# Performance work log

Measured on AMD Instinct MI355X. Metric: run time of the kernel, lower is better.

Reference implementation:

```python
import jax, jax.numpy as jnp
import numpy as np

DT_MIN, DT_MAX, STAB_EPS, RMS_EPS = 1e-4, 10.0, 1e-8, 1e-6


def soft_clamp(x, mn=DT_MIN, mx=DT_MAX):
    center = (mx + mn) / 2.0
    half = (mx - mn) / 2.0
    return center + half * jnp.tanh((x - center) / half)


def setup_inputs() -> dict:
    key = jax.random.key(0)
    ks = jax.random.split(key, 8)
    B, L, D, N = 1, 4096, 1024, 16
    s = D ** -0.5
    x = jax.random.normal(ks[0], (B, L, D), jnp.float32)
    # S4D-real style init: A = -exp(A_log), rows = -(1..N)
    A_log = jnp.broadcast_to(jnp.log(jnp.arange(1, N + 1, dtype=jnp.float32)), (D, N))
    W_delta = jax.random.normal(ks[1], (D, D), jnp.float32) * s
    b_delta = jax.random.normal(ks[2], (D,), jnp.float32) * 0.1
    W_B = jax.random.normal(ks[3], (D, N), jnp.float32) * s
    W_C = jax.random.normal(ks[4], (D, N), jnp.float32) * s
    D_skip = jax.random.normal(ks[5], (D,), jnp.float32) * 0.1 + 1.0
    norm_weight = jnp.ones((D,), jnp.float32)
    return {"x": x, "A_log": A_log, "W_delta": W_delta, "b_delta": b_delta,
            "W_B": W_B, "W_C": W_C, "D_skip": D_skip, "norm_weight": norm_weight}


def reference(x, A_log, W_delta, b_delta, W_B, W_C, D_skip, norm_weight):
    # RMSNorm pre-norm
    rms = jnp.sqrt(jnp.mean(x * x, axis=-1, keepdims=True) + RMS_EPS)
    xn = norm_weight * x / rms                                  # (B, L, D)

    # input-dependent (selective) parameters
    delta = soft_clamp(jax.nn.softplus(xn @ W_delta + b_delta))  # (B, L, D)
    Bp = xn @ W_B                                               # (B, L, N)
    C = xn @ W_C                                                # (B, L, N)
    A = -jnp.exp(A_log)                                         # (D, N)

    # guarded Tustin (bilinear) discretization
    half_dA = 0.5 * delta[..., None] * A                        # (B, L, D, N)
    denom_inv = 1.0 / jnp.maximum(1.0 - half_dA, STAB_EPS)
    A_bar = (1.0 + half_dA) * denom_inv                         # (B, L, D, N)
    B_bar = jnp.sqrt(delta)[..., None] * Bp[:, :, None, :] * denom_inv
    Bx = B_bar * xn[..., None]                                  # (B, L, D, N)

    # linear recurrence h_t = A_bar_t * h_{t-1} + Bx_t ; y_t = sum_n C_t * h_t
    def step(h, inp):
        a_t, bx_t, c_t = inp
        h = a_t * h + bx_t                                      # (B, D, N)
        y_t = jnp.einsum('bdn,bn->bd', h, c_t)
        return h, y_t

    h0 = jnp.zeros((x.shape[0], A.shape[0], A.shape[1]), x.dtype)
    seq = (jnp.moveaxis(A_bar, 1, 0), jnp.moveaxis(Bx, 1, 0), jnp.moveaxis(C, 1, 0))
    _, ys = jax.lax.scan(step, h0, seq)
    y = jnp.moveaxis(ys, 0, 1) + D_skip * xn                    # skip connection
    return y
```

## Files before the change

kernel.cpp:

```cpp
#include <hip/hip_runtime.h>
#include <hip/hip_fp16.h>
#include <cmath>

typedef _Float16 half8 __attribute__((ext_vector_type(8)));
typedef _Float16 half4_t __attribute__((ext_vector_type(4)));
typedef _Float16 half2_t __attribute__((ext_vector_type(2)));
typedef float f32x4 __attribute__((ext_vector_type(4)));
typedef float f32x2 __attribute__((ext_vector_type(2)));

#define LDIM 4096
#define DDIM 1024
#define NSTATE 16
#define NCHUNK 128
#define CLEN 32

#define GLD16(g, l) __builtin_amdgcn_global_load_lds( \
    (const __attribute__((address_space(1))) void*)(g), \
    (__attribute__((address_space(3))) void*)(l), 16, 0, 0)

__global__ __launch_bounds__(256) void k_prep_norm(const float* __restrict__ x,
                                                   const float* __restrict__ nw,
                                                   const float* __restrict__ W,
                                                   const float* __restrict__ WB,
                                                   const float* __restrict__ WC,
                                                   _Float16* __restrict__ xnh,
                                                   _Float16* __restrict__ Wt,
                                                   _Float16* __restrict__ BCe) {
  const int b = blockIdx.x, t = threadIdx.x;
  if (b < 4096) {
    const int l = b;
    float4 v = ((const float4*)(x + (size_t)l * DDIM))[t];
    float ss = v.x * v.x + v.y * v.y + v.z * v.z + v.w * v.w;
#pragma unroll
    for (int off = 32; off; off >>= 1) ss += __shfl_xor(ss, off, 64);
    __shared__ float sred[4];
    if ((t & 63) == 0) sred[t >> 6] = ss;
    __syncthreads();
    float tot = sred[0] + sred[1] + sred[2] + sred[3];
    float r = rsqrtf(tot * (1.0f / (float)DDIM) + 1e-6f);
    float4 wv = ((const float4*)nw)[t];
    half4_t h;
    h[0] = (_Float16)(v.x * wv.x * r); h[1] = (_Float16)(v.y * wv.y * r);
    h[2] = (_Float16)(v.z * wv.z * r); h[3] = (_Float16)(v.w * wv.w * r);
    ((half4_t*)(xnh + (size_t)l * DDIM))[t] = h;
  } else if (b < 4352) {
    __shared__ float tile[64][65];
    const int bb = b - 4096;
    const int n0 = (bb & 15) * 64, k0 = (bb >> 4) * 64;
#pragma unroll
    for (int i = 0; i < 16; ++i) {
      int idx = t + i * 256;
      int kk = idx >> 6, nn = idx & 63;
      tile[kk][nn] = W[(size_t)(k0 + kk) * DDIM + n0 + nn];
    }
    __syncthreads();
#pragma unroll
    for (int i = 0; i < 16; ++i) {
      int idx = t + i * 256;
      int nn = idx >> 6, kk = idx & 63;
      Wt[(size_t)(n0 + nn) * DDIM + k0 + kk] = (_Float16)tile[kk][nn];
    }
  } else {
    const int by2 = b - 4352;
#pragma unroll
    for (int rr = 0; rr < 2; ++rr) {
      int r = 2 * by2 + rr;
      const float* src = (r < 16) ? WB : WC;
      int n = r & 15;
#pragma unroll
      for (int j = 0; j < 4; ++j) {
        int k = t * 4 + j;
        BCe[(size_t)r * DDIM + k] = (_Float16)src[(size_t)k * NSTATE + n];
      }
    }
  }
}

__global__ __launch_bounds__(256, 2) void k_gemm64(const _Float16* __restrict__ Ah,
                                                   const _Float16* __restrict__ Bh,
                                                   const _Float16* __restrict__ B2h,
                                                   const float* __restrict__ b_delta,
                                                   half2_t* __restrict__ sxh,
                                                   float* __restrict__ bpc) {
  __shared__ __align__(16) _Float16 As[2][128 * 64];
  __shared__ __align__(16) _Float16 Bs[2][64 * 64];
  __shared__ __align__(16) _Float16 B2s[2][32 * 64];
  const int t = threadIdx.x;
  const int w = t >> 6, lane = t & 63;
  const int quad = lane >> 4, l16 = lane & 15;
  const int wr = w >> 1, wc = w & 1;
  const int bid = blockIdx.x;
  const int bx = bid & 15, by = bid >> 4;
  const int tileM = by * 128, tileN = bx * 64;
  const int srow = lane >> 3;
  const int sslot = (lane & 7) ^ srow;
  const _Float16* gA0 = Ah + (size_t)(tileM + w * 32 + srow) * DDIM + sslot * 8;
  const _Float16* gB0 = Bh + (size_t)(tileN + w * 16 + srow) * DDIM + sslot * 8;
  const _Float16* gC0 = B2h + (size_t)(w * 8 + srow) * DDIM + sslot * 8;

  f32x4 acc[4][2], acc2[4];
#pragma unroll
  for (int i = 0; i < 4; ++i) {
    acc2[i] = (f32x4){0.f, 0.f, 0.f, 0.f};
#pragma unroll
    for (int j = 0; j < 2; ++j) acc[i][j] = (f32x4){0.f, 0.f, 0.f, 0.f};
  }

  auto stage = [&](int kt, int p) {
    const int ko = kt * 64;
#pragma unroll
    for (int g = 0; g < 4; ++g)
      GLD16(gA0 + (size_t)g * 8 * DDIM + ko, &As[p][(w * 32 + g * 8) * 64]);
#pragma unroll
    for (int g = 0; g < 2; ++g)
      GLD16(gB0 + (size_t)g * 8 * DDIM + ko, &Bs[p][(w * 16 + g * 8) * 64]);
    if (bx == 0)
      GLD16(gC0 + ko, &B2s[p][(w * 8) * 64]);
  };

  stage(0, 0);
  for (int kt = 0; kt < 16; ++kt) {
    const int p = kt & 1;
    __syncthreads();
    if (kt < 15) stage(kt + 1, p ^ 1);
#pragma unroll
    for (int ks = 0; ks < 2; ++ks) {
      const int sw = ((ks * 4 + quad) ^ (l16 & 7)) * 8;
      half8 af[4], bf[2];
#pragma unroll
      for (int i = 0; i < 4; ++i)
        af[i] = *(const half8*)&As[p][(wr * 64 + i * 16 + l16) * 64 + sw];
#pragma unroll
      for (int j = 0; j < 2; ++j)
        bf[j] = *(const half8*)&Bs[p][(wc * 32 + j * 16 + l16) * 64 + sw];
#pragma unroll
      for (int i = 0; i < 4; ++i)
#pragma unroll
        for (int j = 0; j < 2; ++j)
          acc[i][j] = __builtin_amdgcn_mfma_f32_16x16x32_f16(af[i], bf[j], acc[i][j], 0, 0, 0);
      if (bx == 0) {
        half8 cf = *(const half8*)&B2s[p][(wc * 16 + l16) * 64 + sw];
#pragma unroll
        for (int i = 0; i < 4; ++i)
          acc2[i] = __builtin_amdgcn_mfma_f32_16x16x32_f16(af[i], cf, acc2[i], 0, 0, 0);
      }
    }
  }

  const float cC = 5.00005f, cH = 4.99995f, invH = 1.0f / 4.99995f;
  float bdl[2];
#pragma unroll
  for (int j = 0; j < 2; ++j) bdl[j] = b_delta[tileN + wc * 32 + j * 16 + l16];
#pragma unroll
  for (int i = 0; i < 4; ++i) {
#pragma unroll
    for (int r = 0; r < 4; ++r) {
      int row = tileM + wr * 64 + i * 16 + quad * 4 + r;
#pragma unroll
      for (int j = 0; j < 2; ++j) {
        int col = tileN + wc * 32 + j * 16 + l16;
        float z = acc[i][j][r] + bdl[j];
        float e = __expf(-fabsf(z));
        float sp = fmaxf(z, 0.f) + __logf(1.0f + e);
        float tt = (sp - cC) * invH;
        float e2 = __expf(2.0f * tt);
        float th = 1.0f - 2.0f * __builtin_amdgcn_rcpf(e2 + 1.0f);
        float dt = fmaf(cH, th, cC);
        half2_t pk;
        pk[0] = (_Float16)sqrtf(dt);
        pk[1] = Ah[(size_t)row * DDIM + col];
        sxh[(size_t)row * DDIM + col] = pk;
      }
      if (bx == 0)
        bpc[(size_t)row * 32 + wc * 16 + l16] = acc2[i][r];
    }
  }
}

__global__ __launch_bounds__(256) void k_scan1(const half2_t* __restrict__ sxh,
                                               const float* __restrict__ bpc,
                                               const float* __restrict__ A_log,
                                               float2* __restrict__ Ph) {
  const int t = threadIdx.x;
  const int d = blockIdx.x * 256 + t;
  const int c = blockIdx.y;
  const float4* alp = (const float4*)(A_log + (size_t)d * NSTATE);
  f32x2 halfA[8], h[8], P[8];
#pragma unroll
  for (int q = 0; q < 4; ++q) {
    float4 al = alp[q];
    halfA[2 * q + 0] = (f32x2){-0.5f * __expf(al.x), -0.5f * __expf(al.y)};
    halfA[2 * q + 1] = (f32x2){-0.5f * __expf(al.z), -0.5f * __expf(al.w)};
  }
#pragma unroll
  for (int j = 0; j < 8; ++j) { h[j] = (f32x2){0.f, 0.f}; P[j] = (f32x2){1.f, 1.f}; }
  const half2_t* sxr = sxh + (size_t)c * CLEN * DDIM + d;
  const float* bp0 = bpc + (size_t)c * CLEN * 32;
  const f32x2 one2 = {1.f, 1.f}, two2 = {2.f, 2.f}, mone2 = {-1.f, -1.f};
#pragma unroll 4
  for (int i = 0; i < CLEN; ++i) {
    half2_t sx = sxr[(size_t)i * DDIM];
    float sdv = (float)sx[0], xv = (float)sx[1];
    float dsq = sdv * sdv, sdx = sdv * xv;
    f32x2 dsq2 = {dsq, dsq}, sdx2 = {sdx, sdx};
    const float* bp = bp0 + i * 32;
#pragma unroll
    for (int j = 0; j < 8; ++j) {
      f32x2 bB = *(const f32x2*)(bp + 2 * j);
      f32x2 hd = dsq2 * halfA[j];
      f32x2 om = one2 - hd;
      f32x2 di = {__builtin_amdgcn_rcpf(om[0]), __builtin_amdgcn_rcpf(om[1])};
      f32x2 ab = __builtin_elementwise_fma(di, two2, mone2);
      h[j] = __builtin_elementwise_fma(ab, h[j], sdx2 * bB * di);
      P[j] = P[j] * ab;
    }
  }
#pragma unroll
  for (int j = 0; j < 8; ++j) {
    Ph[((size_t)c * NSTATE + 2 * j + 0) * DDIM + d] = make_float2(P[j][0], h[j][0]);
    Ph[((size_t)c * NSTATE + 2 * j + 1) * DDIM + d] = make_float2(P[j][1], h[j][1]);
  }
}

__global__ __launch_bounds__(64) void k_comb(const float2* __restrict__ Ph,
                                             float* __restrict__ Hinit) {
  const int g = blockIdx.x * 64 + threadIdx.x;
  float H = 0.f;
  for (int cb = 0; cb < NCHUNK; cb += 16) {
    float2 ph[16];
#pragma unroll
    for (int u = 0; u < 16; ++u)
      ph[u] = Ph[(size_t)(cb + u) * (DDIM * NSTATE) + g];
#pragma unroll
    for (int u = 0; u < 16; ++u) {
      Hinit[(size_t)(cb + u) * (DDIM * NSTATE) + g] = H;
      H = fmaf(ph[u].x, H, ph[u].y);
    }
  }
}

__global__ __launch_bounds__(256) void k_scan2(const half2_t* __restrict__ sxh,
                                               const float* __restrict__ bpc,
                                               const float* __restrict__ A_log,
                                               const float* __restrict__ Hinit,
                                               const float* __restrict__ Dskip,
                                               float* __restrict__ y) {
  const int t = threadIdx.x;
  const int d = blockIdx.x * 256 + t;
  const int c = blockIdx.y;
  const float4* alp = (const float4*)(A_log + (size_t)d * NSTATE);
  f32x2 halfA[8], h[8];
#pragma unroll
  for (int q = 0; q < 4; ++q) {
    float4 al = alp[q];
    halfA[2 * q + 0] = (f32x2){-0.5f * __expf(al.x), -0.5f * __expf(al.y)};
    halfA[2 * q + 1] = (f32x2){-0.5f * __expf(al.z), -0.5f * __expf(al.w)};
  }
#pragma unroll
  for (int j = 0; j < 8; ++j)
    h[j] = (f32x2){Hinit[(size_t)c * (DDIM * NSTATE) + (size_t)(2 * j) * DDIM + d],
                   Hinit[(size_t)c * (DDIM * NSTATE) + (size_t)(2 * j + 1) * DDIM + d]};
  const float dsk = Dskip[d];
  const half2_t* sxr = sxh + (size_t)c * CLEN * DDIM + d;
  const float* bp0 = bpc + (size_t)c * CLEN * 32;
  float* yr = y + (size_t)c * CLEN * DDIM + d;
  const f32x2 one2 = {1.f, 1.f}, two2 = {2.f, 2.f}, mone2 = {-1.f, -1.f};
#pragma unroll 4
  for (int i = 0; i < CLEN; ++i) {
    half2_t sx = sxr[(size_t)i * DDIM];
    float sdv = (float)sx[0], xv = (float)sx[1];
    float dsq = sdv * sdv, sdx = sdv * xv;
    f32x2 dsq2 = {dsq, dsq}, sdx2 = {sdx, sdx};
    const float* bp = bp0 + i * 32;
    f32x2 acc = {0.f, 0.f};
#pragma unroll
    for (int j = 0; j < 8; ++j) {
      f32x2 bB = *(const f32x2*)(bp + 2 * j);
      f32x2 bC = *(const f32x2*)(bp + 16 + 2 * j);
      f32x2 hd = dsq2 * halfA[j];
      f32x2 om = one2 - hd;
      f32x2 di = {__builtin_amdgcn_rcpf(om[0]), __builtin_amdgcn_rcpf(om[1])};
      f32x2 ab = __builtin_elementwise_fma(di, two2, mone2);
      h[j] = __builtin_elementwise_fma(ab, h[j], sdx2 * bB * di);
      acc = __builtin_elementwise_fma(bC, h[j], acc);
    }
    yr[(size_t)i * DDIM] = fmaf(dsk, xv, acc[0] + acc[1]);
  }
}

extern "C" void kernel_launch(void* const* d_in, const int* in_sizes, int n_in,
                              void* d_out, int out_size, void* d_ws, size_t ws_size,
                              hipStream_t stream) {
  const float* x       = (const float*)d_in[0];
  const float* A_log   = (const float*)d_in[1];
  const float* W_delta = (const float*)d_in[2];
  const float* b_delta = (const float*)d_in[3];
  const float* W_B     = (const float*)d_in[4];
  const float* W_C     = (const float*)d_in[5];
  const float* D_skip  = (const float*)d_in[6];
  const float* norm_w  = (const float*)d_in[7];
  float* y = (float*)d_out;

  char* ws = (char*)d_ws;
  const size_t MB = 1024 * 1024;
  _Float16* xnh = (_Float16*)(ws);
  _Float16* Wt  = (_Float16*)(ws + 8 * MB);
  _Float16* BCe = (_Float16*)(ws + 10 * MB);
  float*    bpc = (float*)(ws + 10 * MB + 512 * 1024);
  half2_t*  sxh = (half2_t*)(ws + 11 * MB);
  float2*   Ph  = (float2*)(ws + 27 * MB);
  float*    Hin = (float*)(ws + 43 * MB);
  (void)ws_size; (void)in_sizes; (void)n_in; (void)out_size;

  hipLaunchKernelGGL(k_prep_norm, dim3(4368), dim3(256), 0, stream,
                     x, norm_w, W_delta, W_B, W_C, xnh, Wt, BCe);
  hipLaunchKernelGGL(k_gemm64, dim3(512), dim3(256), 0, stream,
                     xnh, Wt, BCe, b_delta, sxh, bpc);
  hipLaunchKernelGGL(k_scan1, dim3(4, NCHUNK), dim3(256), 0, stream,
                     sxh, bpc, A_log, Ph);
  hipLaunchKernelGGL(k_comb, dim3(256), dim3(64), 0, stream, Ph, Hin);
  hipLaunchKernelGGL(k_scan2, dim3(4, NCHUNK), dim3(256), 0, stream,
                     sxh, bpc, A_log, Hin, D_skip, y);
}
```

Baseline: 159.5 us.

## Split scan state across four lanes per channel and stage B/C in LDS

The chunked scan kernels now give each channel four threads, each owning four of the sixteen states, which quadruples the thread count (16x128 blocks) and cuts per-thread serial work and registers. The per-chunk B/C projections are staged once into shared memory instead of being read from global memory by every thread. In the second scan, partial outputs are reduced across the four lanes with shuffles. The GEMM block index is also remapped so consecutive blocks share the same N tile across eight M tiles, aiming for better L2 reuse. The cost is redundant sxh loads (four lanes read the same value), extra shuffles per step, and more, smaller blocks.

```diff
diff --git a/kernel.cpp b/kernel.cpp
--- a/kernel.cpp
+++ b/kernel.cpp
@@ -90,7 +90,8 @@
   const int quad = lane >> 4, l16 = lane & 15;
   const int wr = w >> 1, wc = w & 1;
   const int bid = blockIdx.x;
-  const int bx = bid & 15, by = bid >> 4;
+  const int bx = bid >> 5;
+  const int by = (bid & 7) + ((bid >> 3) & 3) * 8;
   const int tileM = by * 128, tileN = bx * 64;
   const int srow = lane >> 3;
   const int sslot = (lane & 7) ^ srow;
@@ -177,25 +178,24 @@
   }
 }
 
-__global__ __launch_bounds__(256) void k_scan1(const half2_t* __restrict__ sxh,
-                                               const float* __restrict__ bpc,
-                                               const float* __restrict__ A_log,
-                                               float2* __restrict__ Ph) {
+__global__ __launch_bounds__(256, 8) void k_scan1(const half2_t* __restrict__ sxh,
+                                                  const float* __restrict__ bpc,
+                                                  const float* __restrict__ A_log,
+                                                  float2* __restrict__ Ph) {
+  __shared__ __align__(16) float bcs[CLEN * 32];
   const int t = threadIdx.x;
-  const int d = blockIdx.x * 256 + t;
+  const int q = t & 3;
+  const int d = blockIdx.x * 64 + (t >> 2);
   const int c = blockIdx.y;
-  const float4* alp = (const float4*)(A_log + (size_t)d * NSTATE);
-  f32x2 halfA[8], h[8], P[8];
-#pragma unroll
-  for (int q = 0; q < 4; ++q) {
-    float4 al = alp[q];
-    halfA[2 * q + 0] = (f32x2){-0.5f * __expf(al.x), -0.5f * __expf(al.y)};
-    halfA[2 * q + 1] = (f32x2){-0.5f * __expf(al.z), -0.5f * __expf(al.w)};
-  }
-#pragma unroll
-  for (int j = 0; j < 8; ++j) { h[j] = (f32x2){0.f, 0.f}; P[j] = (f32x2){1.f, 1.f}; }
+  ((float4*)bcs)[t] = ((const float4*)(bpc + (size_t)c * CLEN * 32))[t];
+  float4 al = *(const float4*)(A_log + (size_t)d * NSTATE + q * 4);
+  f32x2 halfA[2], h[2], P[2];
+  halfA[0] = (f32x2){-0.5f * __expf(al.x), -0.5f * __expf(al.y)};
+  halfA[1] = (f32x2){-0.5f * __expf(al.z), -0.5f * __expf(al.w)};
+  h[0] = h[1] = (f32x2){0.f, 0.f};
+  P[0] = P[1] = (f32x2){1.f, 1.f};
+  __syncthreads();
   const half2_t* sxr = sxh + (size_t)c * CLEN * DDIM + d;
-  const float* bp0 = bpc + (size_t)c * CLEN * 32;
   const f32x2 one2 = {1.f, 1.f}, two2 = {2.f, 2.f}, mone2 = {-1.f, -1.f};
 #pragma unroll 4
   for (int i = 0; i < CLEN; ++i) {
@@ -203,22 +203,22 @@
     float sdv = (float)sx[0], xv = (float)sx[1];
     float dsq = sdv * sdv, sdx = sdv * xv;
     f32x2 dsq2 = {dsq, dsq}, sdx2 = {sdx, sdx};
-    const float* bp = bp0 + i * 32;
-#pragma unroll
-    for (int j = 0; j < 8; ++j) {
-      f32x2 bB = *(const f32x2*)(bp + 2 * j);
+    f32x4 bB = *(const f32x4*)&bcs[i * 32 + q * 4];
+#pragma unroll
+    for (int j = 0; j < 2; ++j) {
+      f32x2 bb = (f32x2){bB[2 * j], bB[2 * j + 1]};
       f32x2 hd = dsq2 * halfA[j];
       f32x2 om = one2 - hd;
       f32x2 di = {__builtin_amdgcn_rcpf(om[0]), __builtin_amdgcn_rcpf(om[1])};
       f32x2 ab = __builtin_elementwise_fma(di, two2, mone2);
-      h[j] = __builtin_elementwise_fma(ab, h[j], sdx2 * bB * di);
+      h[j] = __builtin_elementwise_fma(ab, h[j], sdx2 * bb * di);
       P[j] = P[j] * ab;
     }
   }
 #pragma unroll
-  for (int j = 0; j < 8; ++j) {
-    Ph[((size_t)c * NSTATE + 2 * j + 0) * DDIM + d] = make_float2(P[j][0], h[j][0]);
-    Ph[((size_t)c * NSTATE + 2 * j + 1) * DDIM + d] = make_float2(P[j][1], h[j][1]);
+  for (int j = 0; j < 2; ++j) {
+    Ph[((size_t)c * NSTATE + q * 4 + 2 * j + 0) * DDIM + d] = make_float2(P[j][0], h[j][0]);
+    Ph[((size_t)c * NSTATE + q * 4 + 2 * j + 1) * DDIM + d] = make_float2(P[j][1], h[j][1]);
   }
 }
 
@@ -239,30 +239,28 @@
   }
 }
 
-__global__ __launch_bounds__(256) void k_scan2(const half2_t* __restrict__ sxh,
-                                               const float* __restrict__ bpc,
-                                               const float* __restrict__ A_log,
-                                               const float* __restrict__ Hinit,
-                                               const float* __restrict__ Dskip,
-                                               float* __restrict__ y) {
+__global__ __launch_bounds__(256, 8) void k_scan2(const half2_t* __restrict__ sxh,
+                                                  const float* __restrict__ bpc,
+                                                  const float* __restrict__ A_log,
+                                                  const float* __restrict__ Hinit,
+                                                  const float* __restrict__ Dskip,
+                                                  float* __restrict__ y) {
+  __shared__ __align__(16) float bcs[CLEN * 32];
   const int t = threadIdx.x;
-  const int d = blockIdx.x * 256 + t;
+  const int q = t & 3;
+  const int d = blockIdx.x * 64 + (t >> 2);
   const int c = blockIdx.y;
-  const float4* alp = (const float4*)(A_log + (size_t)d * NSTATE);
-  f32x2 halfA[8], h[8];
-#pragma unroll
-  for (int q = 0; q < 4; ++q) {
-    float4 al = alp[q];
-    halfA[2 * q + 0] = (f32x2){-0.5f * __expf(al.x), -0.5f * __expf(al.y)};
-    halfA[2 * q + 1] = (f32x2){-0.5f * __expf(al.z), -0.5f * __expf(al.w)};
-  }
-#pragma unroll
-  for (int j = 0; j < 8; ++j)
-    h[j] = (f32x2){Hinit[(size_t)c * (DDIM * NSTATE) + (size_t)(2 * j) * DDIM + d],
-                   Hinit[(size_t)c * (DDIM * NSTATE) + (size_t)(2 * j + 1) * DDIM + d]};
+  ((float4*)bcs)[t] = ((const float4*)(bpc + (size_t)c * CLEN * 32))[t];
+  float4 al = *(const float4*)(A_log + (size_t)d * NSTATE + q * 4);
+  f32x2 halfA[2], h[2];
+  halfA[0] = (f32x2){-0.5f * __expf(al.x), -0.5f * __expf(al.y)};
+  halfA[1] = (f32x2){-0.5f * __expf(al.z), -0.5f * __expf(al.w)};
+  const float* hb = Hinit + (size_t)c * (DDIM * NSTATE) + d;
+  h[0] = (f32x2){hb[(size_t)(q * 4 + 0) * DDIM], hb[(size_t)(q * 4 + 1) * DDIM]};
+  h[1] = (f32x2){hb[(size_t)(q * 4 + 2) * DDIM], hb[(size_t)(q * 4 + 3) * DDIM]};
   const float dsk = Dskip[d];
+  __syncthreads();
   const half2_t* sxr = sxh + (size_t)c * CLEN * DDIM + d;
-  const float* bp0 = bpc + (size_t)c * CLEN * 32;
   float* yr = y + (size_t)c * CLEN * DDIM + d;
   const f32x2 one2 = {1.f, 1.f}, two2 = {2.f, 2.f}, mone2 = {-1.f, -1.f};
 #pragma unroll 4
@@ -271,20 +269,24 @@
     float sdv = (float)sx[0], xv = (float)sx[1];
     float dsq = sdv * sdv, sdx = sdv * xv;
     f32x2 dsq2 = {dsq, dsq}, sdx2 = {sdx, sdx};
-    const float* bp = bp0 + i * 32;
+    f32x4 bB = *(const f32x4*)&bcs[i * 32 + q * 4];
+    f32x4 bC = *(const f32x4*)&bcs[i * 32 + 16 + q * 4];
     f32x2 acc = {0.f, 0.f};
 #pragma unroll
-    for (int j = 0; j < 8; ++j) {
-      f32x2 bB = *(const f32x2*)(bp + 2 * j);
-      f32x2 bC = *(const f32x2*)(bp + 16 + 2 * j);
+    for (int j = 0; j < 2; ++j) {
+      f32x2 bb = (f32x2){bB[2 * j], bB[2 * j + 1]};
+      f32x2 cc = (f32x2){bC[2 * j], bC[2 * j + 1]};
       f32x2 hd = dsq2 * halfA[j];
       f32x2 om = one2 - hd;
       f32x2 di = {__builtin_amdgcn_rcpf(om[0]), __builtin_amdgcn_rcpf(om[1])};
       f32x2 ab = __builtin_elementwise_fma(di, two2, mone2);
-      h[j] = __builtin_elementwise_fma(ab, h[j], sdx2 * bB * di);
-      acc = __builtin_elementwise_fma(bC, h[j], acc);
-    }
-    yr[(size_t)i * DDIM] = fmaf(dsk, xv, acc[0] + acc[1]);
+      h[j] = __builtin_elementwise_fma(ab, h[j], sdx2 * bb * di);
+      acc = __builtin_elementwise_fma(cc, h[j], acc);
+    }
+    float a = acc[0] + acc[1];
+    a += __shfl_xor(a, 1, 64);
+    a += __shfl_xor(a, 2, 64);
+    if (q == 0) yr[(size_t)i * DDIM] = fmaf(dsk, xv, a);
   }
 }
 
@@ -316,9 +318,9 @@
                      x, norm_w, W_delta, W_B, W_C, xnh, Wt, BCe);
   hipLaunchKernelGGL(k_gemm64, dim3(512), dim3(256), 0, stream,
                      xnh, Wt, BCe, b_delta, sxh, bpc);
-  hipLaunchKernelGGL(k_scan1, dim3(4, NCHUNK), dim3(256), 0, stream,
+  hipLaunchKernelGGL(k_scan1, dim3(16, NCHUNK), dim3(256), 0, stream,
                      sxh, bpc, A_log, Ph);
   hipLaunchKernelGGL(k_comb, dim3(256), dim3(64), 0, stream, Ph, Hin);
-  hipLaunchKernelGGL(k_scan2, dim3(4, NCHUNK), dim3(256), 0, stream,
+  hipLaunchKernelGGL(k_scan2, dim3(16, NCHUNK), dim3(256), 0, stream,
                      sxh, bpc, A_log, Hin, D_skip, y);
 }
```

Result: no change. 158.5 us (-0.6%).
